# Optimization experiments

Measured on AMD Instinct MI355X. Metric: run time of the kernel, lower is better.

The kernel has to match this reference:

```python
import jax, jax.numpy as jnp
import numpy as np

N = 50000       # nodes
E = 800000      # random edges (self-loops appended in reference)
F_IN = 3        # dataset.num_features
CH = 32         # conv_hidden_channels
HEADS = 4       # attention_heads
C1_OUT = CH * 2     # 64
C2_OUT = CH * 4     # 128
LIN = 256       # lin_hidden_channels
NCLS = 25       # dataset.num_classes


def setup_inputs() -> dict:
    key = jax.random.key(0)
    ks = jax.random.split(key, 20)
    g = lambda k, s: (jax.random.normal(k, s, jnp.float32) * 0.05)
    return {
        "x": jax.random.normal(ks[0], (N, F_IN), jnp.float32),
        "edge_index": jax.random.randint(ks[1], (2, E), 0, N, dtype=jnp.int64),
        # fc0 (Linear stored as [in, out])
        "fc0_w": g(ks[2], (F_IN, CH)), "fc0_b": g(ks[3], (CH,)),
        # FeaStConv 1: in=CH, out=C1_OUT
        "conv1_w": g(ks[4], (CH, HEADS * C1_OUT)),
        "conv1_u": g(ks[5], (CH, HEADS)),
        "conv1_c": g(ks[6], (HEADS,)),
        "conv1_b": g(ks[7], (C1_OUT,)),
        # FeaStConv 2: in=C1_OUT, out=C2_OUT
        "conv2_w": g(ks[8], (C1_OUT, HEADS * C2_OUT)),
        "conv2_u": g(ks[9], (C1_OUT, HEADS)),
        "conv2_c": g(ks[10], (HEADS,)),
        "conv2_b": g(ks[11], (C2_OUT,)),
        # fc1, fc2
        "fc1_w": g(ks[12], (C2_OUT, LIN)), "fc1_b": g(ks[13], (LIN,)),
        "fc2_w": g(ks[14], (LIN, NCLS)), "fc2_b": g(ks[15], (NCLS,)),
    }


def feast_conv(x, src, dst, W, u, c, b):
    """FeaStConv (PyG): q = softmax((x_j - x_i) u + c) over heads,
    msg = sum_h q_h * (x_j W_h), mean-aggregated onto dst nodes."""
    xi = x[dst]                          # [E', in]
    xj = x[src]                          # [E', in]
    q = jax.nn.softmax((xj - xi) @ u + c, axis=-1)   # [E', H]
    m = (xj @ W).reshape(xj.shape[0], HEADS, -1)     # [E', H, out]
    msg = jnp.einsum('eh,ehd->ed', q, m)             # [E', out]
    agg = jax.ops.segment_sum(msg, dst, num_segments=N)
    cnt = jax.ops.segment_sum(jnp.ones((msg.shape[0],), x.dtype), dst,
                              num_segments=N)
    return agg / cnt[:, None] + b


def reference(x, edge_index, fc0_w, fc0_b,
              conv1_w, conv1_u, conv1_c, conv1_b,
              conv2_w, conv2_u, conv2_c, conv2_b,
              fc1_w, fc1_b, fc2_w, fc2_b):
    loops = jnp.arange(N, dtype=edge_index.dtype)
    src = jnp.concatenate([edge_index[0], loops])   # messages flow src -> dst
    dst = jnp.concatenate([edge_index[1], loops])
    h = jax.nn.elu(x @ fc0_w + fc0_b)
    h = jax.nn.elu(feast_conv(h, src, dst, conv1_w, conv1_u, conv1_c, conv1_b))
    h = jax.nn.elu(feast_conv(h, src, dst, conv2_w, conv2_u, conv2_c, conv2_b))
    h = jax.nn.elu(h @ fc1_w + fc1_b)
    # dropout skipped (eval mode / training=self.training)
    out = h @ fc2_w + fc2_b
    return jax.nn.log_softmax(out, axis=1)
```

## Files before the change

### kernel.cpp

```cpp
#include <hip/hip_runtime.h>
#include <math.h>

#define F_IN 3
#define CH 32
#define HEADS 4
#define C1_OUT 64
#define C2_OUT 128
#define LIN 256
#define NCLS 25
#define NBIN 8

typedef __attribute__((ext_vector_type(8))) short bf16x8;
typedef __attribute__((ext_vector_type(4))) float f32x4;

__device__ __forceinline__ float elu_f(float x) {
    return x > 0.f ? x : (__expf(x) - 1.f);
}

__device__ __forceinline__ unsigned short f2bf(float f) {
    union { float f; unsigned int u; } v; v.f = f;
    unsigned int u = v.u + 0x7fffu + ((v.u >> 16) & 1u);
    return (unsigned short)(u >> 16);
}

__device__ __forceinline__ float bf2f(unsigned short u) {
    union { unsigned int u; float f; } v; v.u = ((unsigned int)u) << 16;
    return v.f;
}

__device__ __forceinline__ void unpackq(unsigned lo, unsigned hi, float& x, float& y,
                                        float& z, float& w) {
    x = bf2f((unsigned short)(lo & 0xffffu));
    y = bf2f((unsigned short)(lo >> 16));
    z = bf2f((unsigned short)(hi & 0xffffu));
    w = bf2f((unsigned short)(hi >> 16));
}

__device__ __forceinline__ void softmax4(const float* __restrict__ c,
                                         float& q0, float& q1, float& q2, float& q3) {
    float c0 = c[0], c1 = c[1], c2 = c[2], c3 = c[3];
    float mx = fmaxf(fmaxf(c0, c1), fmaxf(c2, c3));
    float e0 = __expf(c0 - mx), e1 = __expf(c1 - mx);
    float e2 = __expf(c2 - mx), e3 = __expf(c3 - mx);
    float inv = 1.f / (e0 + e1 + e2 + e3);
    q0 = e0 * inv; q1 = e1 * inv; q2 = e2 * inv; q3 = e3 * inv;
}

__device__ __forceinline__ void qslot(const float4* __restrict__ pp, float4 pd,
                                      float c0, float c1, float c2, float c3,
                                      int sx, bool valid,
                                      unsigned& qlo, unsigned& qhi) {
    float4 ps = pp[sx];
    float t0 = ps.x - pd.x + c0;
    float t1 = ps.y - pd.y + c1;
    float t2 = ps.z - pd.z + c2;
    float t3 = ps.w - pd.w + c3;
    float mx = fmaxf(fmaxf(t0, t1), fmaxf(t2, t3));
    float s0 = __expf(t0 - mx), s1 = __expf(t1 - mx);
    float s2 = __expf(t2 - mx), s3 = __expf(t3 - mx);
    float inv = 1.f / (s0 + s1 + s2 + s3);
    qlo = qhi = 0u;
    if (valid) {
        qlo = (unsigned)f2bf(s0 * inv) | ((unsigned)f2bf(s1 * inv) << 16);
        qhi = (unsigned)f2bf(s2 * inv) | ((unsigned)f2bf(s3 * inv) << 16);
    }
}

__global__ __launch_bounds__(256) void k_fc0(
    const float* __restrict__ x, const float* __restrict__ w,
    const float* __restrict__ b, const float* __restrict__ u,
    unsigned short* __restrict__ h0, float* __restrict__ p, int n_nodes) {
    int wid = (blockIdx.x * blockDim.x + threadIdx.x) >> 6;
    int lane = threadIdx.x & 63;
    int half = lane >> 5, c = lane & 31;
    int node = wid * 2 + half;
    if (node >= n_nodes) return;
    float acc = b[c];
#pragma unroll
    for (int i = 0; i < F_IN; ++i) acc += x[node * F_IN + i] * w[i * CH + c];
    unsigned short hb = f2bf(elu_f(acc));
    h0[(size_t)node * CH + c] = hb;
    float hv = bf2f(hb);
    float a0 = hv * u[c * HEADS + 0];
    float a1 = hv * u[c * HEADS + 1];
    float a2 = hv * u[c * HEADS + 2];
    float a3 = hv * u[c * HEADS + 3];
#pragma unroll
    for (int m = 16; m >= 1; m >>= 1) {
        a0 += __shfl_xor(a0, m, 32); a1 += __shfl_xor(a1, m, 32);
        a2 += __shfl_xor(a2, m, 32); a3 += __shfl_xor(a3, m, 32);
    }
    if (c == 0) {
        p[node * 4 + 0] = a0; p[node * 4 + 1] = a1;
        p[node * 4 + 2] = a2; p[node * 4 + 3] = a3;
    }
}

__global__ void k_deg(const int* __restrict__ dst, int* __restrict__ deg,
                      int ne, int npb) {
    int bin = blockIdx.x & (NBIN - 1);
    int blk = blockIdx.x >> 3;
    int nblk = gridDim.x >> 3;
    int per = (ne + nblk - 1) / nblk;
    int start = blk * per;
    int end = start + per < ne ? start + per : ne;
    int lo = bin * npb, hi = lo + npb;
    for (int e = start + threadIdx.x; e < end; e += blockDim.x) {
        int d = dst[e];
        if (d >= lo && d < hi) atomicAdd(&deg[d], 1);
    }
}

#define SCAN_BS 1024
__global__ __launch_bounds__(SCAN_BS) void k_scan_a(
    const int* __restrict__ deg, int* __restrict__ offa,
    int* __restrict__ blksum, int n) {
    __shared__ int buf[SCAN_BS];
    int tid = threadIdx.x;
    int i = blockIdx.x * SCAN_BS + tid;
    int v = (i < n) ? deg[i] : 0;
    buf[tid] = v;
    __syncthreads();
    for (int s = 1; s < SCAN_BS; s <<= 1) {
        int t = (tid >= s) ? buf[tid - s] : 0;
        __syncthreads();
        buf[tid] += t;
        __syncthreads();
    }
    if (i < n) offa[i] = buf[tid] - v;
    if (tid == SCAN_BS - 1) blksum[blockIdx.x] = buf[tid];
}

__global__ void k_scan_b(int* __restrict__ blksum, int* __restrict__ offa,
                         int nblk, int n) {
    int tid = threadIdx.x;
    int orig = (tid < nblk) ? blksum[tid] : 0;
    int v = orig;
#pragma unroll
    for (int s = 1; s < 64; s <<= 1) {
        int t = __shfl_up(v, s, 64);
        if (tid >= s) v += t;
    }
    if (tid < nblk) blksum[tid] = v - orig;
    if (tid == nblk - 1) offa[n] = v;
}

__global__ void k_scan_c(int* __restrict__ offa, int* __restrict__ cur,
                         const int* __restrict__ blksum, int n) {
    int i = blockIdx.x * blockDim.x + threadIdx.x;
    if (i < n) {
        int o = offa[i] + blksum[i >> 10];
        offa[i] = o;
        cur[i] = o;
    }
}

__global__ void k_scatter(const int* __restrict__ eidx, int* __restrict__ cur,
                          int* __restrict__ ssrc, int ne, int npb) {
    int bin = blockIdx.x & (NBIN - 1);
    int blk = blockIdx.x >> 3;
    int nblk = gridDim.x >> 3;
    int per = (ne + nblk - 1) / nblk;
    int start = blk * per;
    int end = start + per < ne ? start + per : ne;
    int lo = bin * npb, hi = lo + npb;
    for (int e = start + threadIdx.x; e < end; e += blockDim.x) {
        int d = eidx[ne + e];
        if (d >= lo && d < hi) {
            int s = eidx[e];
            int pos = atomicAdd(&cur[d], 1);
            ssrc[pos] = s;
        }
    }
}

template<int IN>
__global__ void k_proj(const unsigned short* __restrict__ h,
                       const float* __restrict__ u,
                       float* __restrict__ p, int n_nodes) {
    int node = blockIdx.x * blockDim.x + threadIdx.x;
    if (node >= n_nodes) return;
    const unsigned short* hr = h + (size_t)node * IN;
    float a0 = 0.f, a1 = 0.f, a2 = 0.f, a3 = 0.f;
#pragma unroll
    for (int kb = 0; kb < IN; kb += 8) {
        uint4 uu = *(const uint4*)(hr + kb);
        unsigned int ws_[4] = {uu.x, uu.y, uu.z, uu.w};
#pragma unroll
        for (int j = 0; j < 4; ++j) {
            float vlo = bf2f((unsigned short)(ws_[j] & 0xffffu));
            float vhi = bf2f((unsigned short)(ws_[j] >> 16));
            int k0 = kb + j * 2, k1 = kb + j * 2 + 1;
            a0 = fmaf(vlo, u[k0 * HEADS + 0], a0); a0 = fmaf(vhi, u[k1 * HEADS + 0], a0);
            a1 = fmaf(vlo, u[k0 * HEADS + 1], a1); a1 = fmaf(vhi, u[k1 * HEADS + 1], a1);
            a2 = fmaf(vlo, u[k0 * HEADS + 2], a2); a2 = fmaf(vhi, u[k1 * HEADS + 2], a2);
            a3 = fmaf(vlo, u[k0 * HEADS + 3], a3); a3 = fmaf(vhi, u[k1 * HEADS + 3], a3);
        }
    }
    p[node * 4 + 0] = a0; p[node * 4 + 1] = a1;
    p[node * 4 + 2] = a2; p[node * 4 + 3] = a3;
}

__global__ __launch_bounds__(256) void k_agg1(
    const unsigned short* __restrict__ h, const int* __restrict__ offa,
    const int* __restrict__ ssrc, const float* __restrict__ p,
    const float* __restrict__ cvec, unsigned short* __restrict__ arow,
    int n_nodes) {
    int wid = (blockIdx.x * blockDim.x + threadIdx.x) >> 6;
    int lane = threadIdx.x & 63;
    if (wid >= n_nodes) return;
    int half = lane >> 5, ch = lane & 31;
    int slot = lane & 7, sbase = lane & 56;
    int e0 = __builtin_amdgcn_readfirstlane(offa[wid]);
    int e1 = __builtin_amdgcn_readfirstlane(offa[wid + 1]);
    const float4* pp = (const float4*)p;
    float4 pd = pp[wid];
    float c0 = cvec[0], c1 = cvec[1], c2 = cvec[2], c3 = cvec[3];
    float a0 = 0.f, a1 = 0.f, a2 = 0.f, a3 = 0.f;
    for (int e = e0; e < e1; e += 8) {
        int ee = e + slot;
        int ec = ee < e1 ? ee : e0;
        int sx = ssrc[ec];
        unsigned qlo, qhi;
        qslot(pp, pd, c0, c1, c2, c3, sx, ee < e1, qlo, qhi);
#pragma unroll
        for (int m = 0; m < 4; ++m) {
            int src = sbase + 2 * m + half;
            int sj = __shfl(sx, src, 64);
            unsigned lo = (unsigned)__shfl((int)qlo, src, 64);
            unsigned hi = (unsigned)__shfl((int)qhi, src, 64);
            float xj = bf2f(h[(size_t)sj * CH + ch]);
            float qx, qy, qz, qw;
            unpackq(lo, hi, qx, qy, qz, qw);
            a0 = fmaf(qx, xj, a0); a1 = fmaf(qy, xj, a1);
            a2 = fmaf(qz, xj, a2); a3 = fmaf(qw, xj, a3);
        }
    }
    a0 += __shfl_xor(a0, 32); a1 += __shfl_xor(a1, 32);
    a2 += __shfl_xor(a2, 32); a3 += __shfl_xor(a3, 32);
    if (half == 0) {
        float qc0, qc1, qc2, qc3;
        softmax4(cvec, qc0, qc1, qc2, qc3);
        float xi = bf2f(h[(size_t)wid * CH + ch]);
        a0 = fmaf(qc0, xi, a0); a1 = fmaf(qc1, xi, a1);
        a2 = fmaf(qc2, xi, a2); a3 = fmaf(qc3, xi, a3);
        float inv = 1.f / (float)(e1 - e0 + 1);
        arow[(size_t)wid * 128 + 0 * CH + ch] = f2bf(a0 * inv);
        arow[(size_t)wid * 128 + 1 * CH + ch] = f2bf(a1 * inv);
        arow[(size_t)wid * 128 + 2 * CH + ch] = f2bf(a2 * inv);
        arow[(size_t)wid * 128 + 3 * CH + ch] = f2bf(a3 * inv);
    }
}

__global__ __launch_bounds__(256) void k_agg2(
    const unsigned short* __restrict__ h, const int* __restrict__ offa,
    const int* __restrict__ ssrc, const float* __restrict__ p,
    const float* __restrict__ cvec, unsigned short* __restrict__ arow,
    int n_nodes) {
    int wid = (blockIdx.x * blockDim.x + threadIdx.x) >> 6;
    int lane = threadIdx.x & 63;
    if (wid >= n_nodes) return;
    int slot = lane & 7, sbase = lane & 56;
    int e0 = __builtin_amdgcn_readfirstlane(offa[wid]);
    int e1 = __builtin_amdgcn_readfirstlane(offa[wid + 1]);
    const float4* pp = (const float4*)p;
    float4 pd = pp[wid];
    float c0 = cvec[0], c1 = cvec[1], c2 = cvec[2], c3 = cvec[3];
    float a0 = 0.f, a1 = 0.f, a2 = 0.f, a3 = 0.f;
    for (int e = e0; e < e1; e += 8) {
        int ee = e + slot;
        int ec = ee < e1 ? ee : e0;
        int sx = ssrc[ec];
        unsigned qlo, qhi;
        qslot(pp, pd, c0, c1, c2, c3, sx, ee < e1, qlo, qhi);
#pragma unroll
        for (int j = 0; j < 8; ++j) {
            int src = sbase + j;
            int sj = __shfl(sx, src, 64);
            unsigned lo = (unsigned)__shfl((int)qlo, src, 64);
            unsigned hi = (unsigned)__shfl((int)qhi, src, 64);
            float xj = bf2f(h[(size_t)sj * C1_OUT + lane]);
            float qx, qy, qz, qw;
            unpackq(lo, hi, qx, qy, qz, qw);
            a0 = fmaf(qx, xj, a0); a1 = fmaf(qy, xj, a1);
            a2 = fmaf(qz, xj, a2); a3 = fmaf(qw, xj, a3);
        }
    }
    float qc0, qc1, qc2, qc3;
    softmax4(cvec, qc0, qc1, qc2, qc3);
    float xi = bf2f(h[(size_t)wid * C1_OUT + lane]);
    a0 = fmaf(qc0, xi, a0); a1 = fmaf(qc1, xi, a1);
    a2 = fmaf(qc2, xi, a2); a3 = fmaf(qc3, xi, a3);
    float inv = 1.f / (float)(e1 - e0 + 1);
    arow[(size_t)wid * 256 + 0 * C1_OUT + lane] = f2bf(a0 * inv);
    arow[(size_t)wid * 256 + 1 * C1_OUT + lane] = f2bf(a1 * inv);
    arow[(size_t)wid * 256 + 2 * C1_OUT + lane] = f2bf(a2 * inv);
    arow[(size_t)wid * 256 + 3 * C1_OUT + lane] = f2bf(a3 * inv);
}

__global__ void k_prepAll(const float* __restrict__ W1, unsigned short* __restrict__ B1,
                          const float* __restrict__ W2, unsigned short* __restrict__ B2,
                          const float* __restrict__ Wf, unsigned short* __restrict__ Bf,
                          const float* __restrict__ Wc, unsigned short* __restrict__ Bc) {
    int idx = blockIdx.x * blockDim.x + threadIdx.x;
    if (idx < 8192) {
        int o = idx / 128, j = idx % 128;
        int hh = j / 32, k = j % 32;
        B1[idx] = f2bf(W1[k * (HEADS * 64) + hh * 64 + o]);
    } else if (idx < 40960) {
        int i = idx - 8192;
        int o = i / 256, j = i % 256;
        int hh = j / 64, k = j % 64;
        B2[i] = f2bf(W2[k * (HEADS * 128) + hh * 128 + o]);
    } else if (idx < 73728) {
        int i = idx - 40960;
        int o = i / 128, j = i % 128;
        Bf[i] = f2bf(Wf[j * 256 + o]);
    } else if (idx < 81920) {
        int i = idx - 73728;
        int o = i >> 8, k = i & 255;
        Bc[i] = f2bf(o < NCLS ? Wc[k * NCLS + o] : 0.f);
    }
}

template<int K, int M>
__global__ __launch_bounds__(256) void k_mgemm(
    const unsigned short* __restrict__ A, const unsigned short* __restrict__ Bt,
    const float* __restrict__ bias, unsigned short* __restrict__ D, int n) {
    constexpr int CPW = M / 4;
    constexpr int NCF = CPW / 16;
    constexpr int NKC = K / 32;
    __shared__ unsigned short Al[64 * K];
    int tid = threadIdx.x;
    int w = tid >> 6, l = tid & 63;
    int l16 = l & 15, l4 = l >> 4;
    int rowbase = blockIdx.x * 64;

    bf16x8 bfr[NCF][NKC];
#pragma unroll
    for (int c = 0; c < NCF; ++c)
#pragma unroll
        for (int t = 0; t < NKC; ++t) {
            int col = w * CPW + c * 16 + l16;
            int k = t * 32 + l4 * 8;
            bfr[c][t] = *(const bf16x8*)(Bt + (size_t)col * K + k);
        }

    constexpr int CHUNKS = 64 * K / 8;
    for (int idx = tid; idx < CHUNKS; idx += 256) {
        int row = idx / (K / 8);
        int kb = (idx % (K / 8)) * 8;
        int grow = rowbase + row;
        uint4 u;
        if (grow < n) u = *(const uint4*)(A + (size_t)grow * K + kb);
        else          u.x = u.y = u.z = u.w = 0u;
        int byte = ((row * K + kb) * 2) ^ ((row & 7) << 4);
        *(uint4*)((char*)Al + byte) = u;
    }
    __syncthreads();

#pragma unroll
    for (int r = 0; r < 4; ++r) {
        bf16x8 af[NKC];
        int row = r * 16 + l16;
#pragma unroll
        for (int t = 0; t < NKC; ++t) {
            int byte = ((row * K + t * 32 + l4 * 8) * 2) ^ ((row & 7) << 4);
            af[t] = *(bf16x8*)((char*)Al + byte);
        }
#pragma unroll
        for (int c = 0; c < NCF; ++c) {
            f32x4 acc = {0.f, 0.f, 0.f, 0.f};
#pragma unroll
            for (int t = 0; t < NKC; ++t)
                acc = __builtin_amdgcn_mfma_f32_16x16x32_bf16(af[t], bfr[c][t], acc, 0, 0, 0);
            int col = w * CPW + c * 16 + l16;
            float bv = bias[col];
#pragma unroll
            for (int j = 0; j < 4; ++j) {
                int grow = rowbase + r * 16 + l4 * 4 + j;
                if (grow < n)
                    D[(size_t)grow * M + col] = f2bf(elu_f(acc[j] + bv));
            }
        }
    }
}

__global__ __launch_bounds__(256) void k_head(
    const unsigned short* __restrict__ A, const unsigned short* __restrict__ Btf,
    const float* __restrict__ bias1, const unsigned short* __restrict__ Btc,
    const float* __restrict__ bias2, float* __restrict__ out, int n) {
    __shared__ unsigned short Al[64 * 128];
    __shared__ unsigned short Hl[64 * 256];
    int tid = threadIdx.x;
    int w = tid >> 6, l = tid & 63;
    int l16 = l & 15, l4 = l >> 4;
    int rowbase = blockIdx.x * 64;

    bf16x8 bfr[4][4];
#pragma unroll
    for (int c = 0; c < 4; ++c)
#pragma unroll
        for (int t = 0; t < 4; ++t) {
            int col = w * 64 + c * 16 + l16;
            int k = t * 32 + l4 * 8;
            bfr[c][t] = *(const bf16x8*)(Btf + (size_t)col * 128 + k);
        }

    for (int idx = tid; idx < 1024; idx += 256) {
        int row = idx >> 4;
        int kb = (idx & 15) * 8;
        int grow = rowbase + row;
        uint4 u;
        if (grow < n) u = *(const uint4*)(A + (size_t)grow * 128 + kb);
        else          u.x = u.y = u.z = u.w = 0u;
        int byte = ((row * 128 + kb) * 2) ^ ((row & 7) << 4);
        *(uint4*)((char*)Al + byte) = u;
    }
    __syncthreads();

#pragma unroll
    for (int r = 0; r < 4; ++r) {
        bf16x8 af[4];
        int row = r * 16 + l16;
#pragma unroll
        for (int t = 0; t < 4; ++t) {
            int byte = ((row * 128 + t * 32 + l4 * 8) * 2) ^ ((row & 7) << 4);
            af[t] = *(bf16x8*)((char*)Al + byte);
        }
#pragma unroll
        for (int c = 0; c < 4; ++c) {
            f32x4 acc = {0.f, 0.f, 0.f, 0.f};
#pragma unroll
            for (int t = 0; t < 4; ++t)
                acc = __builtin_amdgcn_mfma_f32_16x16x32_bf16(af[t], bfr[c][t], acc, 0, 0, 0);
            int col = w * 64 + c * 16 + l16;
            float bv = bias1[col];
#pragma unroll
            for (int j = 0; j < 4; ++j) {
                int lrow = r * 16 + l4 * 4 + j;
                unsigned short v = f2bf(elu_f(acc[j] + bv));
                int byte = ((lrow * 256 + col) * 2) ^ ((lrow & 7) << 4);
                *(unsigned short*)((char*)Hl + byte) = v;
            }
        }
    }
    __syncthreads();

    bf16x8 b0[8], b1[8];
#pragma unroll
    for (int t = 0; t < 8; ++t) {
        int k = t * 32 + l4 * 8;
        b0[t] = *(const bf16x8*)(Btc + (size_t)l16 * LIN + k);
        b1[t] = *(const bf16x8*)(Btc + (size_t)(16 + l16) * LIN + k);
    }
    float bb0 = bias2[l16];
    bool hi_ok = (l16 < NCLS - 16);
    float bb1 = hi_ok ? bias2[16 + l16] : 0.f;

    int lrow = w * 16 + l16;
    bf16x8 af[8];
#pragma unroll
    for (int t = 0; t < 8; ++t) {
        int byte = ((lrow * 256 + t * 32 + l4 * 8) * 2) ^ ((lrow & 7) << 4);
        af[t] = *(bf16x8*)((char*)Hl + byte);
    }
    f32x4 acc0 = {0.f, 0.f, 0.f, 0.f}, acc1 = {0.f, 0.f, 0.f, 0.f};
#pragma unroll
    for (int t = 0; t < 8; ++t) {
        acc0 = __builtin_amdgcn_mfma_f32_16x16x32_bf16(af[t], b0[t], acc0, 0, 0, 0);
        acc1 = __builtin_amdgcn_mfma_f32_16x16x32_bf16(af[t], b1[t], acc1, 0, 0, 0);
    }
#pragma unroll
    for (int j = 0; j < 4; ++j) {
        float v0 = acc0[j] + bb0;
        float v1 = acc1[j] + bb1;
        float m = fmaxf(v0, hi_ok ? v1 : -1e30f);
#pragma unroll
        for (int msk = 8; msk >= 1; msk >>= 1)
            m = fmaxf(m, __shfl_xor(m, msk, 16));
        float s = __expf(v0 - m) + (hi_ok ? __expf(v1 - m) : 0.f);
#pragma unroll
        for (int msk = 8; msk >= 1; msk >>= 1)
            s += __shfl_xor(s, msk, 16);
        float lse = m + __logf(s);
        int ro = rowbase + w * 16 + l4 * 4 + j;
        if (ro < n) {
            out[(size_t)ro * NCLS + l16] = v0 - lse;
            if (hi_ok) out[(size_t)ro * NCLS + 16 + l16] = v1 - lse;
        }
    }
}

extern "C" void kernel_launch(void* const* d_in, const int* in_sizes, int n_in,
                              void* d_out, int out_size, void* d_ws, size_t ws_size,
                              hipStream_t stream) {
    const float* x     = (const float*)d_in[0];
    const int*   eidx  = (const int*)d_in[1];
    const float* fc0_w = (const float*)d_in[2];
    const float* fc0_b = (const float*)d_in[3];
    const float* c1w   = (const float*)d_in[4];
    const float* c1u   = (const float*)d_in[5];
    const float* c1c   = (const float*)d_in[6];
    const float* c1b   = (const float*)d_in[7];
    const float* c2w   = (const float*)d_in[8];
    const float* c2u   = (const float*)d_in[9];
    const float* c2c   = (const float*)d_in[10];
    const float* c2b   = (const float*)d_in[11];
    const float* fc1w  = (const float*)d_in[12];
    const float* fc1b  = (const float*)d_in[13];
    const float* fc2w  = (const float*)d_in[14];
    const float* fc2b  = (const float*)d_in[15];

    int n_nodes = in_sizes[0] / F_IN;
    int ne      = in_sizes[1] / 2;

    auto align4 = [](size_t v) { return (v + 3) & ~(size_t)3; };
    float* ws = (float*)d_ws;
    size_t t = 0;
    size_t off_o = t; t += align4((size_t)n_nodes + 1);
    size_t cur_o = t; t += align4((size_t)n_nodes);
    size_t blk_o = t; t += 64;
    size_t p_o   = t; t += align4((size_t)n_nodes * 4);
    size_t h1_o  = t; t += align4((size_t)n_nodes * 32);
    size_t A_o   = t; t += align4((size_t)n_nodes * 128);
    size_t B_o   = t;
    size_t h0_o  = B_o;
    size_t ss_o  = align4(h0_o + (size_t)n_nodes * 16);
    size_t B_end = ss_o + (size_t)ne;
    size_t B_sz  = B_end - B_o;
    size_t h2_sz = (size_t)n_nodes * 64;
    t = B_o + (B_sz > h2_sz ? B_sz : h2_sz);
    size_t bt1_o = t; t += 4096;
    size_t bt2_o = t; t += 16384;
    size_t btf_o = t; t += 16384;
    size_t btc_o = t; t += 4096;

    int*    offa   = (int*)(ws + off_o);
    int*    cur    = (int*)(ws + cur_o);
    int*    blksum = (int*)(ws + blk_o);
    float*  p      = ws + p_o;
    unsigned short* h1    = (unsigned short*)(ws + h1_o);
    unsigned short* arow1 = (unsigned short*)(ws + A_o);
    unsigned short* arow2 = (unsigned short*)(ws + A_o);
    unsigned short* h0    = (unsigned short*)(ws + h0_o);
    int*    ssrc   = (int*)(ws + ss_o);
    unsigned short* h2    = (unsigned short*)(ws + B_o);
    unsigned short* bt1 = (unsigned short*)(ws + bt1_o);
    unsigned short* bt2 = (unsigned short*)(ws + bt2_o);
    unsigned short* btf = (unsigned short*)(ws + btf_o);
    unsigned short* btc = (unsigned short*)(ws + btc_o);
    float*  out    = (float*)d_out;

    int nblk = (n_nodes + SCAN_BS - 1) / SCAN_BS;
    int npb  = (n_nodes + NBIN - 1) / NBIN;

    k_prepAll<<<(81920 + 255) / 256, 256, 0, stream>>>(c1w, bt1, c2w, bt2, fc1w, btf, fc2w, btc);
    hipMemsetAsync(cur, 0, (size_t)n_nodes * sizeof(int), stream);

    k_fc0<<<(n_nodes * 32 + 255) / 256, 256, 0, stream>>>(x, fc0_w, fc0_b, c1u, h0, p, n_nodes);
    k_deg<<<NBIN * 512, 256, 0, stream>>>(eidx + ne, cur, ne, npb);
    k_scan_a<<<nblk, SCAN_BS, 0, stream>>>(cur, offa, blksum, n_nodes);
    k_scan_b<<<1, 64, 0, stream>>>(blksum, offa, nblk, n_nodes);
    k_scan_c<<<(n_nodes + 255) / 256, 256, 0, stream>>>(offa, cur, blksum, n_nodes);
    k_scatter<<<NBIN * 512, 256, 0, stream>>>(eidx, cur, ssrc, ne, npb);

    int ngrid = (n_nodes + 63) / 64;

    k_agg1<<<(n_nodes * 64 + 255) / 256, 256, 0, stream>>>(h0, offa, ssrc, p, c1c, arow1, n_nodes);
    k_mgemm<128, 64><<<ngrid, 256, 0, stream>>>(arow1, bt1, c1b, h1, n_nodes);

    k_proj<C1_OUT><<<(n_nodes + 255) / 256, 256, 0, stream>>>(h1, c2u, p, n_nodes);
    k_agg2<<<(n_nodes * 64 + 255) / 256, 256, 0, stream>>>(h1, offa, ssrc, p, c2c, arow2, n_nodes);
    k_mgemm<256, 128><<<ngrid, 256, 0, stream>>>(arow2, bt2, c2b, h2, n_nodes);

    k_head<<<ngrid, 256, 0, stream>>>(h2, btf, fc1b, btc, fc2b, out, n_nodes);
}
```

Measured before the change: 234.4 us.

## Fuse edge aggregation with per-conv MFMA GEMM and merge scan passes

Each FeaStConv's neighbour aggregation now writes its 64-row tile of aggregated features straight into shared memory, and the same block then runs the bf16 MFMA GEMM with bias and ELU. This removes the global round trip of the intermediate aggregate rows and one launch per conv layer. The scan's block-sum pass is folded into k_scan_a through a last-block-done atomic counter, dropping a separate tiny launch. The cost is that each wave now handles 8 nodes serially, so there are fewer waves in flight to hide gather latency, and the degree-skewed node loops can leave the GEMM phase waiting at the barrier.

```diff
diff --git a/kernel.cpp b/kernel.cpp
--- a/kernel.cpp
+++ b/kernel.cpp
@@ -114,8 +114,9 @@
 #define SCAN_BS 1024
 __global__ __launch_bounds__(SCAN_BS) void k_scan_a(
     const int* __restrict__ deg, int* __restrict__ offa,
-    int* __restrict__ blksum, int n) {
+    int* __restrict__ blksum, int* __restrict__ done, int n, int nblk) {
     __shared__ int buf[SCAN_BS];
+    __shared__ int lastflag;
     int tid = threadIdx.x;
     int i = blockIdx.x * SCAN_BS + tid;
     int v = (i < n) ? deg[i] : 0;
@@ -128,21 +129,24 @@
         __syncthreads();
     }
     if (i < n) offa[i] = buf[tid] - v;
-    if (tid == SCAN_BS - 1) blksum[blockIdx.x] = buf[tid];
-}
-
-__global__ void k_scan_b(int* __restrict__ blksum, int* __restrict__ offa,
-                         int nblk, int n) {
-    int tid = threadIdx.x;
-    int orig = (tid < nblk) ? blksum[tid] : 0;
-    int v = orig;
-#pragma unroll
-    for (int s = 1; s < 64; s <<= 1) {
-        int t = __shfl_up(v, s, 64);
-        if (tid >= s) v += t;
-    }
-    if (tid < nblk) blksum[tid] = v - orig;
-    if (tid == nblk - 1) offa[n] = v;
+    if (tid == SCAN_BS - 1) atomicExch(&blksum[blockIdx.x], buf[tid]);
+    __threadfence();
+    __syncthreads();
+    if (tid == 0) lastflag = (atomicAdd(done, 1) == nblk - 1) ? 1 : 0;
+    __syncthreads();
+    if (lastflag) {
+        int vv = (tid < nblk) ? atomicAdd(&blksum[tid], 0) : 0;
+        buf[tid] = vv;
+        __syncthreads();
+        for (int s = 1; s < SCAN_BS; s <<= 1) {
+            int t = (tid >= s) ? buf[tid - s] : 0;
+            __syncthreads();
+            buf[tid] += t;
+            __syncthreads();
+        }
+        if (tid < nblk) blksum[tid] = buf[tid] - vv;
+        if (tid == nblk - 1) offa[n] = buf[tid];
+    }
 }
 
 __global__ void k_scan_c(int* __restrict__ offa, int* __restrict__ cur,
@@ -201,108 +205,13 @@
     p[node * 4 + 2] = a2; p[node * 4 + 3] = a3;
 }
 
-__global__ __launch_bounds__(256) void k_agg1(
-    const unsigned short* __restrict__ h, const int* __restrict__ offa,
-    const int* __restrict__ ssrc, const float* __restrict__ p,
-    const float* __restrict__ cvec, unsigned short* __restrict__ arow,
-    int n_nodes) {
-    int wid = (blockIdx.x * blockDim.x + threadIdx.x) >> 6;
-    int lane = threadIdx.x & 63;
-    if (wid >= n_nodes) return;
-    int half = lane >> 5, ch = lane & 31;
-    int slot = lane & 7, sbase = lane & 56;
-    int e0 = __builtin_amdgcn_readfirstlane(offa[wid]);
-    int e1 = __builtin_amdgcn_readfirstlane(offa[wid + 1]);
-    const float4* pp = (const float4*)p;
-    float4 pd = pp[wid];
-    float c0 = cvec[0], c1 = cvec[1], c2 = cvec[2], c3 = cvec[3];
-    float a0 = 0.f, a1 = 0.f, a2 = 0.f, a3 = 0.f;
-    for (int e = e0; e < e1; e += 8) {
-        int ee = e + slot;
-        int ec = ee < e1 ? ee : e0;
-        int sx = ssrc[ec];
-        unsigned qlo, qhi;
-        qslot(pp, pd, c0, c1, c2, c3, sx, ee < e1, qlo, qhi);
-#pragma unroll
-        for (int m = 0; m < 4; ++m) {
-            int src = sbase + 2 * m + half;
-            int sj = __shfl(sx, src, 64);
-            unsigned lo = (unsigned)__shfl((int)qlo, src, 64);
-            unsigned hi = (unsigned)__shfl((int)qhi, src, 64);
-            float xj = bf2f(h[(size_t)sj * CH + ch]);
-            float qx, qy, qz, qw;
-            unpackq(lo, hi, qx, qy, qz, qw);
-            a0 = fmaf(qx, xj, a0); a1 = fmaf(qy, xj, a1);
-            a2 = fmaf(qz, xj, a2); a3 = fmaf(qw, xj, a3);
-        }
-    }
-    a0 += __shfl_xor(a0, 32); a1 += __shfl_xor(a1, 32);
-    a2 += __shfl_xor(a2, 32); a3 += __shfl_xor(a3, 32);
-    if (half == 0) {
-        float qc0, qc1, qc2, qc3;
-        softmax4(cvec, qc0, qc1, qc2, qc3);
-        float xi = bf2f(h[(size_t)wid * CH + ch]);
-        a0 = fmaf(qc0, xi, a0); a1 = fmaf(qc1, xi, a1);
-        a2 = fmaf(qc2, xi, a2); a3 = fmaf(qc3, xi, a3);
-        float inv = 1.f / (float)(e1 - e0 + 1);
-        arow[(size_t)wid * 128 + 0 * CH + ch] = f2bf(a0 * inv);
-        arow[(size_t)wid * 128 + 1 * CH + ch] = f2bf(a1 * inv);
-        arow[(size_t)wid * 128 + 2 * CH + ch] = f2bf(a2 * inv);
-        arow[(size_t)wid * 128 + 3 * CH + ch] = f2bf(a3 * inv);
-    }
-}
-
-__global__ __launch_bounds__(256) void k_agg2(
-    const unsigned short* __restrict__ h, const int* __restrict__ offa,
-    const int* __restrict__ ssrc, const float* __restrict__ p,
-    const float* __restrict__ cvec, unsigned short* __restrict__ arow,
-    int n_nodes) {
-    int wid = (blockIdx.x * blockDim.x + threadIdx.x) >> 6;
-    int lane = threadIdx.x & 63;
-    if (wid >= n_nodes) return;
-    int slot = lane & 7, sbase = lane & 56;
-    int e0 = __builtin_amdgcn_readfirstlane(offa[wid]);
-    int e1 = __builtin_amdgcn_readfirstlane(offa[wid + 1]);
-    const float4* pp = (const float4*)p;
-    float4 pd = pp[wid];
-    float c0 = cvec[0], c1 = cvec[1], c2 = cvec[2], c3 = cvec[3];
-    float a0 = 0.f, a1 = 0.f, a2 = 0.f, a3 = 0.f;
-    for (int e = e0; e < e1; e += 8) {
-        int ee = e + slot;
-        int ec = ee < e1 ? ee : e0;
-        int sx = ssrc[ec];
-        unsigned qlo, qhi;
-        qslot(pp, pd, c0, c1, c2, c3, sx, ee < e1, qlo, qhi);
-#pragma unroll
-        for (int j = 0; j < 8; ++j) {
-            int src = sbase + j;
-            int sj = __shfl(sx, src, 64);
-            unsigned lo = (unsigned)__shfl((int)qlo, src, 64);
-            unsigned hi = (unsigned)__shfl((int)qhi, src, 64);
-            float xj = bf2f(h[(size_t)sj * C1_OUT + lane]);
-            float qx, qy, qz, qw;
-            unpackq(lo, hi, qx, qy, qz, qw);
-            a0 = fmaf(qx, xj, a0); a1 = fmaf(qy, xj, a1);
-            a2 = fmaf(qz, xj, a2); a3 = fmaf(qw, xj, a3);
-        }
-    }
-    float qc0, qc1, qc2, qc3;
-    softmax4(cvec, qc0, qc1, qc2, qc3);
-    float xi = bf2f(h[(size_t)wid * C1_OUT + lane]);
-    a0 = fmaf(qc0, xi, a0); a1 = fmaf(qc1, xi, a1);
-    a2 = fmaf(qc2, xi, a2); a3 = fmaf(qc3, xi, a3);
-    float inv = 1.f / (float)(e1 - e0 + 1);
-    arow[(size_t)wid * 256 + 0 * C1_OUT + lane] = f2bf(a0 * inv);
-    arow[(size_t)wid * 256 + 1 * C1_OUT + lane] = f2bf(a1 * inv);
-    arow[(size_t)wid * 256 + 2 * C1_OUT + lane] = f2bf(a2 * inv);
-    arow[(size_t)wid * 256 + 3 * C1_OUT + lane] = f2bf(a3 * inv);
-}
-
 __global__ void k_prepAll(const float* __restrict__ W1, unsigned short* __restrict__ B1,
                           const float* __restrict__ W2, unsigned short* __restrict__ B2,
                           const float* __restrict__ Wf, unsigned short* __restrict__ Bf,
-                          const float* __restrict__ Wc, unsigned short* __restrict__ Bc) {
+                          const float* __restrict__ Wc, unsigned short* __restrict__ Bc,
+                          int* __restrict__ done) {
     int idx = blockIdx.x * blockDim.x + threadIdx.x;
+    if (idx == 0) *done = 0;
     if (idx < 8192) {
         int o = idx / 128, j = idx % 128;
         int hh = j / 32, k = j % 32;
@@ -323,65 +232,179 @@
     }
 }
 
-template<int K, int M>
-__global__ __launch_bounds__(256) void k_mgemm(
-    const unsigned short* __restrict__ A, const unsigned short* __restrict__ Bt,
+__global__ __launch_bounds__(512) void k_conv1(
+    const unsigned short* __restrict__ h, const int* __restrict__ offa,
+    const int* __restrict__ ssrc, const float* __restrict__ p,
+    const float* __restrict__ cvec, const unsigned short* __restrict__ Bt,
     const float* __restrict__ bias, unsigned short* __restrict__ D, int n) {
-    constexpr int CPW = M / 4;
-    constexpr int NCF = CPW / 16;
-    constexpr int NKC = K / 32;
-    __shared__ unsigned short Al[64 * K];
+    __shared__ unsigned short Al[64 * 128];
     int tid = threadIdx.x;
-    int w = tid >> 6, l = tid & 63;
-    int l16 = l & 15, l4 = l >> 4;
+    int w = tid >> 6, lane = tid & 63;
+    int l16 = lane & 15, l4 = lane >> 4;
     int rowbase = blockIdx.x * 64;
-
-    bf16x8 bfr[NCF][NKC];
-#pragma unroll
-    for (int c = 0; c < NCF; ++c)
-#pragma unroll
-        for (int t = 0; t < NKC; ++t) {
-            int col = w * CPW + c * 16 + l16;
-            int k = t * 32 + l4 * 8;
-            bfr[c][t] = *(const bf16x8*)(Bt + (size_t)col * K + k);
-        }
-
-    constexpr int CHUNKS = 64 * K / 8;
-    for (int idx = tid; idx < CHUNKS; idx += 256) {
-        int row = idx / (K / 8);
-        int kb = (idx % (K / 8)) * 8;
-        int grow = rowbase + row;
-        uint4 u;
-        if (grow < n) u = *(const uint4*)(A + (size_t)grow * K + kb);
-        else          u.x = u.y = u.z = u.w = 0u;
-        int byte = ((row * K + kb) * 2) ^ ((row & 7) << 4);
-        *(uint4*)((char*)Al + byte) = u;
-    }
-    __syncthreads();
-
+    int half = lane >> 5, ch = lane & 31;
+    int slot = lane & 7, sbase = lane & 56;
+    const float4* pp = (const float4*)p;
+    float c0 = cvec[0], c1 = cvec[1], c2 = cvec[2], c3 = cvec[3];
+    float qc0, qc1, qc2, qc3;
+    softmax4(cvec, qc0, qc1, qc2, qc3);
+
+    for (int i = 0; i < 8; ++i) {
+        int lrow = w * 8 + i;
+        int node = rowbase + lrow;
+        if (node >= n) break;
+        int e0 = __builtin_amdgcn_readfirstlane(offa[node]);
+        int e1 = __builtin_amdgcn_readfirstlane(offa[node + 1]);
+        float4 pd = pp[node];
+        float a0 = 0.f, a1 = 0.f, a2 = 0.f, a3 = 0.f;
+        for (int e = e0; e < e1; e += 8) {
+            int ee = e + slot;
+            int ec = ee < e1 ? ee : e0;
+            int sx = ssrc[ec];
+            unsigned qlo, qhi;
+            qslot(pp, pd, c0, c1, c2, c3, sx, ee < e1, qlo, qhi);
+#pragma unroll
+            for (int m = 0; m < 4; ++m) {
+                int src = sbase + 2 * m + half;
+                int sj = __shfl(sx, src, 64);
+                unsigned lo = (unsigned)__shfl((int)qlo, src, 64);
+                unsigned hi = (unsigned)__shfl((int)qhi, src, 64);
+                float xj = bf2f(h[(size_t)sj * CH + ch]);
+                float qx, qy, qz, qw;
+                unpackq(lo, hi, qx, qy, qz, qw);
+                a0 = fmaf(qx, xj, a0); a1 = fmaf(qy, xj, a1);
+                a2 = fmaf(qz, xj, a2); a3 = fmaf(qw, xj, a3);
+            }
+        }
+        a0 += __shfl_xor(a0, 32); a1 += __shfl_xor(a1, 32);
+        a2 += __shfl_xor(a2, 32); a3 += __shfl_xor(a3, 32);
+        if (half == 0) {
+            float xi = bf2f(h[(size_t)node * CH + ch]);
+            a0 = fmaf(qc0, xi, a0); a1 = fmaf(qc1, xi, a1);
+            a2 = fmaf(qc2, xi, a2); a3 = fmaf(qc3, xi, a3);
+            float inv = 1.f / (float)(e1 - e0 + 1);
+            float av[4] = {a0 * inv, a1 * inv, a2 * inv, a3 * inv};
+#pragma unroll
+            for (int q = 0; q < 4; ++q) {
+                int colq = q * CH + ch;
+                int byte = ((lrow * 128 + colq) * 2) ^ ((lrow & 7) << 4);
+                *(unsigned short*)((char*)Al + byte) = f2bf(av[q]);
+            }
+        }
+    }
+    __syncthreads();
+
+    bf16x8 bfr[4];
+    int col = (w & 3) * 16 + l16;
+#pragma unroll
+    for (int t = 0; t < 4; ++t)
+        bfr[t] = *(const bf16x8*)(Bt + (size_t)col * 128 + t * 32 + l4 * 8);
+    float bv = bias[col];
+    int rbase = (w >> 2) * 2;
+#pragma unroll
+    for (int rr = 0; rr < 2; ++rr) {
+        int r = rbase + rr;
+        bf16x8 af[4];
+        int row = r * 16 + l16;
+#pragma unroll
+        for (int t = 0; t < 4; ++t) {
+            int byte = ((row * 128 + t * 32 + l4 * 8) * 2) ^ ((row & 7) << 4);
+            af[t] = *(bf16x8*)((char*)Al + byte);
+        }
+        f32x4 acc = {0.f, 0.f, 0.f, 0.f};
+#pragma unroll
+        for (int t = 0; t < 4; ++t)
+            acc = __builtin_amdgcn_mfma_f32_16x16x32_bf16(af[t], bfr[t], acc, 0, 0, 0);
+#pragma unroll
+        for (int j = 0; j < 4; ++j) {
+            int grow = rowbase + r * 16 + l4 * 4 + j;
+            if (grow < n)
+                D[(size_t)grow * 64 + col] = f2bf(elu_f(acc[j] + bv));
+        }
+    }
+}
+
+__global__ __launch_bounds__(512) void k_conv2(
+    const unsigned short* __restrict__ h, const int* __restrict__ offa,
+    const int* __restrict__ ssrc, const float* __restrict__ p,
+    const float* __restrict__ cvec, const unsigned short* __restrict__ Bt,
+    const float* __restrict__ bias, unsigned short* __restrict__ D, int n) {
+    __shared__ unsigned short Al[64 * 256];
+    int tid = threadIdx.x;
+    int w = tid >> 6, lane = tid & 63;
+    int l16 = lane & 15, l4 = lane >> 4;
+    int rowbase = blockIdx.x * 64;
+    int slot = lane & 7, sbase = lane & 56;
+    const float4* pp = (const float4*)p;
+    float c0 = cvec[0], c1 = cvec[1], c2 = cvec[2], c3 = cvec[3];
+    float qc0, qc1, qc2, qc3;
+    softmax4(cvec, qc0, qc1, qc2, qc3);
+
+    for (int i = 0; i < 8; ++i) {
+        int lrow = w * 8 + i;
+        int node = rowbase + lrow;
+        if (node >= n) break;
+        int e0 = __builtin_amdgcn_readfirstlane(offa[node]);
+        int e1 = __builtin_amdgcn_readfirstlane(offa[node + 1]);
+        float4 pd = pp[node];
+        float a0 = 0.f, a1 = 0.f, a2 = 0.f, a3 = 0.f;
+        for (int e = e0; e < e1; e += 8) {
+            int ee = e + slot;
+            int ec = ee < e1 ? ee : e0;
+            int sx = ssrc[ec];
+            unsigned qlo, qhi;
+            qslot(pp, pd, c0, c1, c2, c3, sx, ee < e1, qlo, qhi);
+#pragma unroll
+            for (int j = 0; j < 8; ++j) {
+                int src = sbase + j;
+                int sj = __shfl(sx, src, 64);
+                unsigned lo = (unsigned)__shfl((int)qlo, src, 64);
+                unsigned hi = (unsigned)__shfl((int)qhi, src, 64);
+                float xj = bf2f(h[(size_t)sj * C1_OUT + lane]);
+                float qx, qy, qz, qw;
+                unpackq(lo, hi, qx, qy, qz, qw);
+                a0 = fmaf(qx, xj, a0); a1 = fmaf(qy, xj, a1);
+                a2 = fmaf(qz, xj, a2); a3 = fmaf(qw, xj, a3);
+            }
+        }
+        float xi = bf2f(h[(size_t)node * C1_OUT + lane]);
+        a0 = fmaf(qc0, xi, a0); a1 = fmaf(qc1, xi, a1);
+        a2 = fmaf(qc2, xi, a2); a3 = fmaf(qc3, xi, a3);
+        float inv = 1.f / (float)(e1 - e0 + 1);
+        float av[4] = {a0 * inv, a1 * inv, a2 * inv, a3 * inv};
+#pragma unroll
+        for (int q = 0; q < 4; ++q) {
+            int colq = q * C1_OUT + lane;
+            int byte = ((lrow * 256 + colq) * 2) ^ ((lrow & 7) << 4);
+            *(unsigned short*)((char*)Al + byte) = f2bf(av[q]);
+        }
+    }
+    __syncthreads();
+
+    bf16x8 bfr[8];
+    int col = w * 16 + l16;
+#pragma unroll
+    for (int t = 0; t < 8; ++t)
+        bfr[t] = *(const bf16x8*)(Bt + (size_t)col * 256 + t * 32 + l4 * 8);
+    float bv = bias[col];
 #pragma unroll
     for (int r = 0; r < 4; ++r) {
-        bf16x8 af[NKC];
+        bf16x8 af[8];
         int row = r * 16 + l16;
 #pragma unroll
-        for (int t = 0; t < NKC; ++t) {
-            int byte = ((row * K + t * 32 + l4 * 8) * 2) ^ ((row & 7) << 4);
+        for (int t = 0; t < 8; ++t) {
+            int byte = ((row * 256 + t * 32 + l4 * 8) * 2) ^ ((row & 7) << 4);
             af[t] = *(bf16x8*)((char*)Al + byte);
         }
-#pragma unroll
-        for (int c = 0; c < NCF; ++c) {
-            f32x4 acc = {0.f, 0.f, 0.f, 0.f};
-#pragma unroll
-            for (int t = 0; t < NKC; ++t)
-                acc = __builtin_amdgcn_mfma_f32_16x16x32_bf16(af[t], bfr[c][t], acc, 0, 0, 0);
-            int col = w * CPW + c * 16 + l16;
-            float bv = bias[col];
-#pragma unroll
-            for (int j = 0; j < 4; ++j) {
-                int grow = rowbase + r * 16 + l4 * 4 + j;
-                if (grow < n)
-                    D[(size_t)grow * M + col] = f2bf(elu_f(acc[j] + bv));
-            }
+        f32x4 acc = {0.f, 0.f, 0.f, 0.f};
+#pragma unroll
+        for (int t = 0; t < 8; ++t)
+            acc = __builtin_amdgcn_mfma_f32_16x16x32_bf16(af[t], bfr[t], acc, 0, 0, 0);
+#pragma unroll
+        for (int j = 0; j < 4; ++j) {
+            int grow = rowbase + r * 16 + l4 * 4 + j;
+            if (grow < n)
+                D[(size_t)grow * 128 + col] = f2bf(elu_f(acc[j] + bv));
         }
     }
 }
@@ -521,16 +544,12 @@
     size_t off_o = t; t += align4((size_t)n_nodes + 1);
     size_t cur_o = t; t += align4((size_t)n_nodes);
     size_t blk_o = t; t += 64;
+    size_t don_o = t; t += 4;
     size_t p_o   = t; t += align4((size_t)n_nodes * 4);
     size_t h1_o  = t; t += align4((size_t)n_nodes * 32);
-    size_t A_o   = t; t += align4((size_t)n_nodes * 128);
-    size_t B_o   = t;
-    size_t h0_o  = B_o;
-    size_t ss_o  = align4(h0_o + (size_t)n_nodes * 16);
-    size_t B_end = ss_o + (size_t)ne;
-    size_t B_sz  = B_end - B_o;
-    size_t h2_sz = (size_t)n_nodes * 64;
-    t = B_o + (B_sz > h2_sz ? B_sz : h2_sz);
+    size_t h2_o  = t; t += align4((size_t)n_nodes * 64);
+    size_t h0_o  = t; t += align4((size_t)n_nodes * 16);
+    size_t ss_o  = t; t += align4((size_t)ne);
     size_t bt1_o = t; t += 4096;
     size_t bt2_o = t; t += 16384;
     size_t btf_o = t; t += 16384;
@@ -539,13 +558,12 @@
     int*    offa   = (int*)(ws + off_o);
     int*    cur    = (int*)(ws + cur_o);
     int*    blksum = (int*)(ws + blk_o);
+    int*    done   = (int*)(ws + don_o);
     float*  p      = ws + p_o;
-    unsigned short* h1    = (unsigned short*)(ws + h1_o);
-    unsigned short* arow1 = (unsigned short*)(ws + A_o);
-    unsigned short* arow2 = (unsigned short*)(ws + A_o);
-    unsigned short* h0    = (unsigned short*)(ws + h0_o);
+    unsigned short* h1  = (unsigned short*)(ws + h1_o);
+    unsigned short* h2  = (unsigned short*)(ws + h2_o);
+    unsigned short* h0  = (unsigned short*)(ws + h0_o);
     int*    ssrc   = (int*)(ws + ss_o);
-    unsigned short* h2    = (unsigned short*)(ws + B_o);
     unsigned short* bt1 = (unsigned short*)(ws + bt1_o);
     unsigned short* bt2 = (unsigned short*)(ws + bt2_o);
     unsigned short* btf = (unsigned short*)(ws + btf_o);
@@ -555,24 +573,21 @@
     int nblk = (n_nodes + SCAN_BS - 1) / SCAN_BS;
     int npb  = (n_nodes + NBIN - 1) / NBIN;
 
-    k_prepAll<<<(81920 + 255) / 256, 256, 0, stream>>>(c1w, bt1, c2w, bt2, fc1w, btf, fc2w, btc);
+    k_prepAll<<<(81920 + 255) / 256, 256, 0, stream>>>(c1w, bt1, c2w, bt2, fc1w, btf, fc2w, btc, done);
     hipMemsetAsync(cur, 0, (size_t)n_nodes * sizeof(int), stream);
 
     k_fc0<<<(n_nodes * 32 + 255) / 256, 256, 0, stream>>>(x, fc0_w, fc0_b, c1u, h0, p, n_nodes);
     k_deg<<<NBIN * 512, 256, 0, stream>>>(eidx + ne, cur, ne, npb);
-    k_scan_a<<<nblk, SCAN_BS, 0, stream>>>(cur, offa, blksum, n_nodes);
-    k_scan_b<<<1, 64, 0, stream>>>(blksum, offa, nblk, n_nodes);
+    k_scan_a<<<nblk, SCAN_BS, 0, stream>>>(cur, offa, blksum, done, n_nodes, nblk);
     k_scan_c<<<(n_nodes + 255) / 256, 256, 0, stream>>>(offa, cur, blksum, n_nodes);
     k_scatter<<<NBIN * 512, 256, 0, stream>>>(eidx, cur, ssrc, ne, npb);
 
     int ngrid = (n_nodes + 63) / 64;
 
-    k_agg1<<<(n_nodes * 64 + 255) / 256, 256, 0, stream>>>(h0, offa, ssrc, p, c1c, arow1, n_nodes);
-    k_mgemm<128, 64><<<ngrid, 256, 0, stream>>>(arow1, bt1, c1b, h1, n_nodes);
+    k_conv1<<<ngrid, 512, 0, stream>>>(h0, offa, ssrc, p, c1c, bt1, c1b, h1, n_nodes);
 
     k_proj<C1_OUT><<<(n_nodes + 255) / 256, 256, 0, stream>>>(h1, c2u, p, n_nodes);
-    k_agg2<<<(n_nodes * 64 + 255) / 256, 256, 0, stream>>>(h1, offa, ssrc, p, c2c, arow2, n_nodes);
-    k_mgemm<256, 128><<<ngrid, 256, 0, stream>>>(arow2, bt2, c2b, h2, n_nodes);
+    k_conv2<<<ngrid, 512, 0, stream>>>(h1, offa, ssrc, p, c2c, bt2, c2b, h2, n_nodes);
 
     k_head<<<ngrid, 256, 0, stream>>>(h2, btf, fc1b, btc, fc2b, out, n_nodes);
 }
```

Result: slower. 271.8 us (+16.0%).
